# Kernel optimization log

Measured on AMD Instinct MI355X. Metric: run time of the kernel, lower is better.

The kernel has to match this reference:

```python
import jax, jax.numpy as jnp
import numpy as np

T = 4096          # total packed tokens
SEG = 512         # segment length (position_ids reset every SEG)
D = 768           # hidden_size
H = 12            # num_attention_heads
DH = D // H       # head_dim = 64
THETA = 160000.0  # global_rope_theta (layer_id=0 -> global attention)


def setup_inputs() -> dict:
    key = jax.random.key(0)
    k1, k2, k3 = jax.random.split(key, 3)
    hidden_states = jax.random.normal(k1, (T, D), dtype=jnp.float32)
    # torch Linear weights stored transposed: here [in, out] for x @ W
    Wqkv = jax.random.normal(k2, (D, 3 * D), dtype=jnp.float32) / np.sqrt(D).astype(np.float32)
    Wo = jax.random.normal(k3, (D, D), dtype=jnp.float32) / np.sqrt(D).astype(np.float32)
    # packed batch: 8 segments of length SEG, position ids restart at 0
    position_ids = (jnp.arange(T, dtype=jnp.int32) % SEG)
    return {"hidden_states": hidden_states, "Wqkv": Wqkv, "Wo": Wo,
            "position_ids": position_ids}


def _neox_rope(x, pos):
    # x: [T, H, DH]; neox-style rotary over full head_dim
    half = DH // 2
    inv_freq = 1.0 / (THETA ** (jnp.arange(half, dtype=jnp.float32) * 2.0 / DH))
    freqs = pos.astype(jnp.float32)[:, None] * inv_freq[None, :]   # [T, half]
    cos = jnp.cos(freqs)[:, None, :]                               # [T, 1, half]
    sin = jnp.sin(freqs)[:, None, :]
    x1, x2 = x[..., :half], x[..., half:]
    return jnp.concatenate([x1 * cos - x2 * sin, x2 * cos + x1 * sin], axis=-1)


def reference(hidden_states, Wqkv, Wo, position_ids):
    qkv = hidden_states @ Wqkv                         # [T, 3D]
    q, k, v = jnp.split(qkv, 3, axis=-1)
    q = q.reshape(T, H, DH)
    k = k.reshape(T, H, DH)
    v = v.reshape(T, H, DH)
    q = _neox_rope(q, position_ids)
    k = _neox_rope(k, position_ids)
    # segment id per token (position_ids==0 marks a new sequence)
    seg = jnp.cumsum((position_ids == 0).astype(jnp.int32)) - 1
    mask = seg[:, None] == seg[None, :]                # block-diagonal [T, T]
    scale = 1.0 / np.sqrt(DH).astype(np.float32)
    scores = jnp.einsum('thd,shd->hts', q, k) * scale  # [H, T, T]
    scores = jnp.where(mask[None, :, :], scores, jnp.float32(-1e30))
    attn = jax.nn.softmax(scores, axis=-1)
    out = jnp.einsum('hts,shd->thd', attn, v).reshape(T, D)
    return out @ Wo
```

## Files before the change

### kernel.cpp

```cpp
#include <hip/hip_runtime.h>
#include <hip/hip_bf16.h>
#include <math.h>

#define T_TOK 4096
#define D_MODEL 768
#define H_HEADS 12
#define DH 64
#define SEG 512
#define NSEG 8
#define QKV_LD 2304

typedef __bf16 bf16x8_t __attribute__((ext_vector_type(8)));
typedef float f32x4_t __attribute__((ext_vector_type(4)));
typedef float f32x16_t __attribute__((ext_vector_type(16)));

#define GBK 64
#define QSCALE 0.18033688011112042f

#define FENCED_BARRIER()                         \
    do {                                         \
        __builtin_amdgcn_sched_barrier(0);       \
        __builtin_amdgcn_s_barrier();            \
        __builtin_amdgcn_sched_barrier(0);       \
    } while (0)

__device__ __forceinline__ void tconv_body(const float* __restrict__ in,
                                           __hip_bfloat16* __restrict__ out,
                                           int N, int K, int bx, int by, int tid,
                                           float (*tile)[65]) {
    const int k0 = by * 64;
    const int n0 = bx * 64;
    const int rr = tid >> 4;
    const int cc = (tid & 15) * 4;
#pragma unroll
    for (int i = 0; i < 4; ++i) {
        int r = i * 16 + rr;
        float4 v = *(const float4*)(in + (size_t)(k0 + r) * N + n0 + cc);
        tile[r][cc] = v.x; tile[r][cc + 1] = v.y; tile[r][cc + 2] = v.z; tile[r][cc + 3] = v.w;
    }
    __syncthreads();
#pragma unroll
    for (int i = 0; i < 4; ++i) {
        int n = i * 16 + rr;
        union { __hip_bfloat16 h[4]; ushort4 u; } o;
        o.h[0] = __float2bfloat16(tile[cc + 0][n]);
        o.h[1] = __float2bfloat16(tile[cc + 1][n]);
        o.h[2] = __float2bfloat16(tile[cc + 2][n]);
        o.h[3] = __float2bfloat16(tile[cc + 3][n]);
        *(ushort4*)(out + (size_t)(n0 + n) * K + k0 + cc) = o.u;
    }
}

__global__ __launch_bounds__(256) void prep_inputs(const float* __restrict__ hidden,
                                                   const float* __restrict__ Wqkv,
                                                   const float* __restrict__ Wo,
                                                   const int* __restrict__ pos_ids,
                                                   __hip_bfloat16* __restrict__ Xb,
                                                   __hip_bfloat16* __restrict__ Wqkvt,
                                                   __hip_bfloat16* __restrict__ Wot,
                                                   float2* __restrict__ rtab) {
    __shared__ float tile[64][65];
    const int b = blockIdx.x;
    const int tid = threadIdx.x;
    if (b < 3072) {
        int i = b * 256 + tid;
        float4 v = ((const float4*)hidden)[i];
        union { __hip_bfloat16 h[4]; ushort4 u; } o;
        o.h[0] = __float2bfloat16(v.x); o.h[1] = __float2bfloat16(v.y);
        o.h[2] = __float2bfloat16(v.z); o.h[3] = __float2bfloat16(v.w);
        ((ushort4*)Xb)[i] = o.u;
    } else if (b < 3504) {
        int lb = b - 3072;
        tconv_body(Wqkv, Wqkvt, QKV_LD, D_MODEL, lb % 36, lb / 36, tid, tile);
    } else if (b < 3648) {
        int lb = b - 3504;
        tconv_body(Wo, Wot, D_MODEL, D_MODEL, lb % 12, lb / 12, tid, tile);
    } else {
        int idx = (b - 3648) * 256 + tid;
        int t = idx >> 5;
        int i = idx & 31;
        float pos = (float)pos_ids[t];
        float inv_freq = powf(160000.0f, -(float)i / 32.0f);
        float s, c;
        sincosf(pos * inv_freq, &s, &c);
        rtab[idx] = make_float2(c, s);
    }
}

__global__ __launch_bounds__(256) void gemm_qkv_fused(const __hip_bfloat16* __restrict__ A,
                                                      const __hip_bfloat16* __restrict__ Bt,
                                                      const float2* __restrict__ rtab,
                                                      __hip_bfloat16* __restrict__ Qb,
                                                      __hip_bfloat16* __restrict__ Kb,
                                                      __hip_bfloat16* __restrict__ Vtb) {
    __shared__ __hip_bfloat16 As[2][64 * GBK];
    __shared__ __hip_bfloat16 Bs[2][128 * GBK];
    const int tid = threadIdx.x;
    const int lane = tid & 63;
    const int wid = tid >> 6;
    const int wr = wid >> 1;
    const int wc = wid & 1;
    const int orig = blockIdx.y * 18 + blockIdx.x;
    const int wg = (orig & 7) * 144 + (orig >> 3);
    const int m0 = (wg / 18) * 64;
    const int n0 = (wg % 18) * 128;
    const int K = D_MODEL;

    f32x4_t acc[2][4];
#pragma unroll
    for (int i = 0; i < 2; ++i)
#pragma unroll
        for (int j = 0; j < 4; ++j) acc[i][j] = (f32x4_t){0.f, 0.f, 0.f, 0.f};

    const int lr = lane >> 3;
    const int gc = lane & 7;
    const int swzc = (gc ^ lr) << 3;
    const int fr = lane & 15;
    const int l4 = lane >> 4;
    const int fsw = fr & 7;

#define STAGE_Q(buf_, k0_)                                                            \
    do {                                                                              \
        _Pragma("unroll")                                                             \
        for (int i_ = 0; i_ < 2; ++i_) {                                              \
            const int row_ = wid * 16 + i_ * 8;                                       \
            const __hip_bfloat16* ga_ = A + (size_t)(m0 + row_ + lr) * K + (k0_) + swzc; \
            __builtin_amdgcn_global_load_lds(                                         \
                (const __attribute__((address_space(1))) void*)ga_,                   \
                (__attribute__((address_space(3))) void*)(As[buf_] + row_ * GBK), 16, 0, 0); \
        }                                                                             \
        _Pragma("unroll")                                                             \
        for (int i_ = 0; i_ < 4; ++i_) {                                              \
            const int row_ = wid * 32 + i_ * 8;                                       \
            const __hip_bfloat16* gb_ = Bt + (size_t)(n0 + row_ + lr) * K + (k0_) + swzc; \
            __builtin_amdgcn_global_load_lds(                                         \
                (const __attribute__((address_space(1))) void*)gb_,                   \
                (__attribute__((address_space(3))) void*)(Bs[buf_] + row_ * GBK), 16, 0, 0); \
        }                                                                             \
    } while (0)

    const int NKT = K / GBK;
    STAGE_Q(0, 0);
    for (int kt = 0; kt < NKT; ++kt) {
        const int cur = kt & 1;
        if (kt < NKT - 1) {
            STAGE_Q(cur ^ 1, (kt + 1) * GBK);
            asm volatile("s_waitcnt vmcnt(6)" ::: "memory");
        } else {
            asm volatile("s_waitcnt vmcnt(0)" ::: "memory");
        }
        FENCED_BARRIER();
#pragma unroll
        for (int kk = 0; kk < 2; ++kk) {
            const int rg = ((kk * 4 + l4) ^ fsw) << 3;
            bf16x8_t af[2], bfr[4];
#pragma unroll
            for (int mi = 0; mi < 2; ++mi)
                af[mi] = *(const bf16x8_t*)(As[cur] + (wr * 32 + mi * 16 + fr) * GBK + rg);
#pragma unroll
            for (int ni = 0; ni < 4; ++ni)
                bfr[ni] = *(const bf16x8_t*)(Bs[cur] + (wc * 64 + ni * 16 + fr) * GBK + rg);
#pragma unroll
            for (int mi = 0; mi < 2; ++mi)
#pragma unroll
                for (int ni = 0; ni < 4; ++ni)
                    acc[mi][ni] = __builtin_amdgcn_mfma_f32_16x16x32_bf16(
                        af[mi], bfr[ni], acc[mi][ni], 0, 0, 0);
        }
        asm volatile("" ::: "memory");
        FENCED_BARRIER();
    }
#undef STAGE_Q

    const int colbase = n0 + wc * 64;
    const int chunk = colbase >> 6;
    const int part = chunk / H_HEADS;
    const int h = chunk % H_HEADS;
    const int trow0 = m0 + wr * 32;

    if (part == 2) {
        const int seg = trow0 >> 9;
        const int key0 = (trow0 & 511) + l4 * 4;
        __hip_bfloat16* vdst = Vtb + ((size_t)(h * NSEG + seg) * DH) * SEG;
#pragma unroll
        for (int mi = 0; mi < 2; ++mi)
#pragma unroll
            for (int ni = 0; ni < 4; ++ni) {
                int d = ni * 16 + fr;
                union { __hip_bfloat16 h2[4]; ushort4 u; } o;
#pragma unroll
                for (int j = 0; j < 4; ++j) o.h2[j] = __float2bfloat16(acc[mi][ni][j]);
                *(ushort4*)(vdst + (size_t)d * SEG + key0 + mi * 16) = o.u;
            }
    } else {
        __hip_bfloat16* dst = (part == 0) ? Qb : Kb;
        const float scale = (part == 0) ? QSCALE : 1.0f;
#pragma unroll
        for (int mi = 0; mi < 2; ++mi)
#pragma unroll
            for (int j = 0; j < 4; ++j) {
                int t = trow0 + mi * 16 + l4 * 4 + j;
                const float2* tb = rtab + (size_t)t * 32;
                float2 cs0 = tb[fr];
                float2 cs1 = tb[16 + fr];
                __hip_bfloat16* op = dst + ((size_t)h * T_TOK + t) * DH;
                float x1, x2;
                x1 = acc[mi][0][j]; x2 = acc[mi][2][j];
                op[fr]      = __float2bfloat16((x1 * cs0.x - x2 * cs0.y) * scale);
                op[fr + 32] = __float2bfloat16((x2 * cs0.x + x1 * cs0.y) * scale);
                x1 = acc[mi][1][j]; x2 = acc[mi][3][j];
                op[16 + fr] = __float2bfloat16((x1 * cs1.x - x2 * cs1.y) * scale);
                op[48 + fr] = __float2bfloat16((x2 * cs1.x + x1 * cs1.y) * scale);
            }
    }
}

__global__ __launch_bounds__(256) void gemm_wo64(const __hip_bfloat16* __restrict__ A,
                                                 const __hip_bfloat16* __restrict__ Bt,
                                                 float* __restrict__ C) {
    __shared__ __hip_bfloat16 As[2][64 * GBK];
    __shared__ __hip_bfloat16 Bs[2][64 * GBK];
    const int tid = threadIdx.x;
    const int lane = tid & 63;
    const int wid = tid >> 6;
    const int wr = wid >> 1, wc = wid & 1;
    const int orig = blockIdx.y * 12 + blockIdx.x;
    const int wg = (orig & 7) * 96 + (orig >> 3);
    const int m0 = (wg / 12) * 64;
    const int n0 = (wg % 12) * 64;
    const int K = D_MODEL;
    const int N = D_MODEL;

    f32x4_t acc[2][2];
#pragma unroll
    for (int i = 0; i < 2; ++i)
#pragma unroll
        for (int j = 0; j < 2; ++j) acc[i][j] = (f32x4_t){0.f, 0.f, 0.f, 0.f};

    const int lr = lane >> 3;
    const int gc = lane & 7;
    const int swzc = (gc ^ lr) << 3;
    const int fr = lane & 15;
    const int l4 = lane >> 4;
    const int fsw = fr & 7;

#define STAGE_W(buf_, k0_)                                                            \
    do {                                                                              \
        _Pragma("unroll")                                                             \
        for (int i_ = 0; i_ < 2; ++i_) {                                              \
            const int row_ = i_ * 32 + wid * 8;                                       \
            const __hip_bfloat16* ga_ = A + (size_t)(m0 + row_ + lr) * K + (k0_) + swzc; \
            __builtin_amdgcn_global_load_lds(                                         \
                (const __attribute__((address_space(1))) void*)ga_,                   \
                (__attribute__((address_space(3))) void*)(As[buf_] + row_ * GBK), 16, 0, 0); \
            const __hip_bfloat16* gb_ = Bt + (size_t)(n0 + row_ + lr) * K + (k0_) + swzc; \
            __builtin_amdgcn_global_load_lds(                                         \
                (const __attribute__((address_space(1))) void*)gb_,                   \
                (__attribute__((address_space(3))) void*)(Bs[buf_] + row_ * GBK), 16, 0, 0); \
        }                                                                             \
    } while (0)

    const int NKT = K / GBK;
    STAGE_W(0, 0);
    for (int kt = 0; kt < NKT; ++kt) {
        const int cur = kt & 1;
        if (kt < NKT - 1) {
            STAGE_W(cur ^ 1, (kt + 1) * GBK);
            asm volatile("s_waitcnt vmcnt(4)" ::: "memory");
        } else {
            asm volatile("s_waitcnt vmcnt(0)" ::: "memory");
        }
        FENCED_BARRIER();
#pragma unroll
        for (int kk = 0; kk < 2; ++kk) {
            const int rg = ((kk * 4 + l4) ^ fsw) << 3;
            bf16x8_t af[2], bfr[2];
#pragma unroll
            for (int mi = 0; mi < 2; ++mi)
                af[mi] = *(const bf16x8_t*)(As[cur] + (wr * 32 + mi * 16 + fr) * GBK + rg);
#pragma unroll
            for (int ni = 0; ni < 2; ++ni)
                bfr[ni] = *(const bf16x8_t*)(Bs[cur] + (wc * 32 + ni * 16 + fr) * GBK + rg);
#pragma unroll
            for (int mi = 0; mi < 2; ++mi)
#pragma unroll
                for (int ni = 0; ni < 2; ++ni)
                    acc[mi][ni] = __builtin_amdgcn_mfma_f32_16x16x32_bf16(
                        af[mi], bfr[ni], acc[mi][ni], 0, 0, 0);
        }
        asm volatile("" ::: "memory");
        FENCED_BARRIER();
    }
#undef STAGE_W

    float* Cb = C + (size_t)(m0 + wr * 32) * N + n0 + wc * 32;
#pragma unroll
    for (int mi = 0; mi < 2; ++mi)
#pragma unroll
        for (int ni = 0; ni < 2; ++ni)
#pragma unroll
            for (int j = 0; j < 4; ++j) {
                int r = mi * 16 + (lane >> 4) * 4 + j;
                Cb[(size_t)r * N + ni * 16 + fr] = acc[mi][ni][j];
            }
}

__device__ __forceinline__ unsigned pk2(float a, float b) {
    unsigned ua = (unsigned)__bfloat16_as_ushort(__float2bfloat16(a));
    unsigned ub = (unsigned)__bfloat16_as_ushort(__float2bfloat16(b));
    return ua | (ub << 16);
}

__global__ __launch_bounds__(256) void attn_mfma(const __hip_bfloat16* __restrict__ Qb,
                                                 const __hip_bfloat16* __restrict__ Kb,
                                                 const __hip_bfloat16* __restrict__ Vtb,
                                                 __hip_bfloat16* __restrict__ attnb) {
    __shared__ __hip_bfloat16 KS[2][64 * 64];
    __shared__ __hip_bfloat16 VS[2][64 * 64];

    const int tid = threadIdx.x;
    const int lane = tid & 63;
    const int w = tid >> 6;
    const int qw = w & 1;
    const int par = w >> 1;
    const int hi = lane >> 5;
    const int l31 = lane & 31;
    const int orig = blockIdx.x;
    const int wg = (orig & 7) * 96 + (orig >> 3);
    const int qt = wg & 7;
    const int hs = wg >> 3;
    const int h = hs % H_HEADS;
    const int seg = hs / H_HEADS;
    const int t0 = seg * SEG + qt * 64 + qw * 32;

    const __hip_bfloat16* kb = Kb + ((size_t)h * T_TOK + seg * SEG) * DH;
    const __hip_bfloat16* vb = Vtb + (size_t)(h * NSEG + seg) * DH * SEG;

    bf16x8_t qf[4];
    {
        const __hip_bfloat16* qp = Qb + ((size_t)h * T_TOK + t0 + l31) * DH + hi * 8;
#pragma unroll
        for (int s = 0; s < 4; ++s) qf[s] = *(const bf16x8_t*)(qp + s * 16);
    }

    const int gr = lane >> 3;
    const int gc = lane & 7;

    f32x16_t ot[2];
#pragma unroll
    for (int n = 0; n < 2; ++n)
#pragma unroll
        for (int r = 0; r < 16; ++r) ot[n][r] = 0.f;
    float lrun = 0.f;

    for (int it = 0; it < 4; ++it) {
        const int tile = 2 * it + par;
#pragma unroll
        for (int i = 0; i < 4; ++i) {
            int G = i * 128 + qw * 64;
            int rk = (G >> 3) + gr;
            const __hip_bfloat16* sk = kb + (size_t)(tile * 64 + rk) * DH + ((gc ^ (rk & 7)) << 3);
            __builtin_amdgcn_global_load_lds(
                (const __attribute__((address_space(1))) void*)sk,
                (__attribute__((address_space(3))) void*)(&KS[par][G * 8]), 16, 0, 0);
            const __hip_bfloat16* sv = vb + (size_t)rk * SEG + tile * 64 + ((gc ^ (rk & 7)) << 3);
            __builtin_amdgcn_global_load_lds(
                (const __attribute__((address_space(1))) void*)sv,
                (__attribute__((address_space(3))) void*)(&VS[par][G * 8]), 16, 0, 0);
        }
        asm volatile("s_waitcnt vmcnt(0)" ::: "memory");
        FENCED_BARRIER();

        f32x16_t st[2];
#pragma unroll
        for (int t = 0; t < 2; ++t)
#pragma unroll
            for (int r = 0; r < 16; ++r) st[t][r] = 0.f;
#pragma unroll
        for (int s = 0; s < 4; ++s) {
            int gk = s * 2 + hi;
            bf16x8_t k0 = *(const bf16x8_t*)(&KS[par][l31 * 64 + ((gk ^ (l31 & 7)) << 3)]);
            bf16x8_t k1 = *(const bf16x8_t*)(&KS[par][(32 + l31) * 64 + ((gk ^ (l31 & 7)) << 3)]);
            st[0] = __builtin_amdgcn_mfma_f32_32x32x16_bf16(k0, qf[s], st[0], 0, 0, 0);
            st[1] = __builtin_amdgcn_mfma_f32_32x32x16_bf16(k1, qf[s], st[1], 0, 0, 0);
        }

        float psum = 0.f;
#pragma unroll
        for (int t = 0; t < 2; ++t)
#pragma unroll
            for (int r = 0; r < 16; ++r) {
                float p = exp2f(st[t][r]);
                st[t][r] = p;
                psum += p;
            }
        psum += __shfl_xor(psum, 32);
        lrun += psum;

        bf16x8_t pf[4];
#pragma unroll
        for (int t = 0; t < 2; ++t) {
            unsigned wv[8], ov[8];
#pragma unroll
            for (int j = 0; j < 8; ++j) wv[j] = pk2(st[t][2 * j], st[t][2 * j + 1]);
#pragma unroll
            for (int j = 0; j < 8; ++j) ov[j] = (unsigned)__shfl_xor((int)wv[j], 32);
#pragma unroll
            for (int sh = 0; sh < 2; ++sh) {
                int b = sh * 4;
                union { unsigned u[4]; bf16x8_t v; } u8;
                u8.u[0] = hi ? ov[b + 2] : wv[b + 0];
                u8.u[1] = hi ? ov[b + 3] : wv[b + 1];
                u8.u[2] = hi ? wv[b + 2] : ov[b + 0];
                u8.u[3] = hi ? wv[b + 3] : ov[b + 1];
                pf[t * 2 + sh] = u8.v;
            }
        }

#pragma unroll
        for (int s = 0; s < 4; ++s) {
            int gk = s * 2 + hi;
            bf16x8_t v0 = *(const bf16x8_t*)(&VS[par][l31 * 64 + ((gk ^ (l31 & 7)) << 3)]);
            bf16x8_t v1 = *(const bf16x8_t*)(&VS[par][(32 + l31) * 64 + ((gk ^ (l31 & 7)) << 3)]);
            ot[0] = __builtin_amdgcn_mfma_f32_32x32x16_bf16(v0, pf[s], ot[0], 0, 0, 0);
            ot[1] = __builtin_amdgcn_mfma_f32_32x32x16_bf16(v1, pf[s], ot[1], 0, 0, 0);
        }
        FENCED_BARRIER();
    }

    float* redO = (float*)KS;
    float* redL = (float*)VS;
    if (par == 1) {
#pragma unroll
        for (int n = 0; n < 2; ++n)
#pragma unroll
            for (int r = 0; r < 16; ++r)
                redO[(qw * 32 + n * 16 + r) * 64 + lane] = ot[n][r];
        redL[qw * 64 + lane] = lrun;
    }
    FENCED_BARRIER();
    if (par == 1) return;
#pragma unroll
    for (int n = 0; n < 2; ++n)
#pragma unroll
        for (int r = 0; r < 16; ++r)
            ot[n][r] += redO[(qw * 32 + n * 16 + r) * 64 + lane];
    lrun += redL[qw * 64 + lane];

    float invl = 1.0f / lrun;
    ushort* Os = (ushort*)VS + 256 + qw * 2112;
#pragma unroll
    for (int n = 0; n < 2; ++n)
#pragma unroll
        for (int r = 0; r < 16; ++r) {
            int d = n * 32 + (r & 3) + 8 * (r >> 2) + 4 * hi;
            Os[d * 33 + l31] = __bfloat16_as_ushort(__float2bfloat16(ot[n][r] * invl));
        }
    {
        unsigned ow2[16];
#pragma unroll
        for (int j = 0; j < 16; ++j) {
            unsigned lo = Os[(hi * 32 + 2 * j) * 33 + l31];
            unsigned hh = Os[(hi * 32 + 2 * j + 1) * 33 + l31];
            ow2[j] = lo | (hh << 16);
        }
        uint4* gd = (uint4*)(attnb + (size_t)(t0 + l31) * D_MODEL + h * DH + hi * 32);
        gd[0] = make_uint4(ow2[0], ow2[1], ow2[2], ow2[3]);
        gd[1] = make_uint4(ow2[4], ow2[5], ow2[6], ow2[7]);
        gd[2] = make_uint4(ow2[8], ow2[9], ow2[10], ow2[11]);
        gd[3] = make_uint4(ow2[12], ow2[13], ow2[14], ow2[15]);
    }
}

extern "C" void kernel_launch(void* const* d_in, const int* in_sizes, int n_in,
                              void* d_out, int out_size, void* d_ws, size_t ws_size,
                              hipStream_t stream) {
    const float* hidden = (const float*)d_in[0];
    const float* Wqkv   = (const float*)d_in[1];
    const float* Wo     = (const float*)d_in[2];
    const int*   pos    = (const int*)d_in[3];

    char* ws = (char*)d_ws;
    __hip_bfloat16* Xb    = (__hip_bfloat16*)(ws);
    __hip_bfloat16* Wqkvt = (__hip_bfloat16*)(ws + 6291456);
    __hip_bfloat16* Wot   = (__hip_bfloat16*)(ws + 9830400);
    __hip_bfloat16* Qb    = (__hip_bfloat16*)(ws + 11010048);
    __hip_bfloat16* Kb    = (__hip_bfloat16*)(ws + 17301504);
    __hip_bfloat16* Vtb   = (__hip_bfloat16*)(ws + 23592960);
    __hip_bfloat16* attnb = (__hip_bfloat16*)(ws + 29884416);
    float2* rtab          = (float2*)(ws + 36175872);
    float* out = (float*)d_out;

    prep_inputs<<<4160, 256, 0, stream>>>(hidden, Wqkv, Wo, pos, Xb, Wqkvt, Wot, rtab);

    gemm_qkv_fused<<<dim3(18, T_TOK / 64), 256, 0, stream>>>(
        Xb, Wqkvt, rtab, Qb, Kb, Vtb);

    attn_mfma<<<768, 256, 0, stream>>>(Qb, Kb, Vtb, attnb);

    gemm_wo64<<<dim3(D_MODEL / 64, T_TOK / 64), 256, 0, stream>>>(
        attnb, Wot, out);
}
```

Measured before the change: 65.87 us.

## Load QKV GEMM A-fragments directly from global into registers, bypassing LDS

```diff
diff --git a/kernel.cpp b/kernel.cpp
--- a/kernel.cpp
+++ b/kernel.cpp
@@ -93,7 +93,6 @@
                                                       __hip_bfloat16* __restrict__ Qb,
                                                       __hip_bfloat16* __restrict__ Kb,
                                                       __hip_bfloat16* __restrict__ Vtb) {
-    __shared__ __hip_bfloat16 As[2][64 * GBK];
     __shared__ __hip_bfloat16 Bs[2][128 * GBK];
     const int tid = threadIdx.x;
     const int lane = tid & 63;
@@ -119,16 +118,19 @@
     const int l4 = lane >> 4;
     const int fsw = fr & 7;
 
-#define STAGE_Q(buf_, k0_)                                                            \
+    const __hip_bfloat16* a0 = A + (size_t)(m0 + wr * 32 + fr) * K + l4 * 8;
+    const __hip_bfloat16* a1 = a0 + (size_t)16 * K;
+
+#define LOAD_AF(dst_, kt_)                                            \
+    do {                                                              \
+        dst_[0][0] = *(const bf16x8_t*)(a0 + (kt_) * GBK);            \
+        dst_[0][1] = *(const bf16x8_t*)(a0 + (kt_) * GBK + 32);       \
+        dst_[1][0] = *(const bf16x8_t*)(a1 + (kt_) * GBK);            \
+        dst_[1][1] = *(const bf16x8_t*)(a1 + (kt_) * GBK + 32);       \
+    } while (0)
+
+#define STAGE_B(buf_, k0_)                                                            \
     do {                                                                              \
-        _Pragma("unroll")                                                             \
-        for (int i_ = 0; i_ < 2; ++i_) {                                              \
-            const int row_ = wid * 16 + i_ * 8;                                       \
-            const __hip_bfloat16* ga_ = A + (size_t)(m0 + row_ + lr) * K + (k0_) + swzc; \
-            __builtin_amdgcn_global_load_lds(                                         \
-                (const __attribute__((address_space(1))) void*)ga_,                   \
-                (__attribute__((address_space(3))) void*)(As[buf_] + row_ * GBK), 16, 0, 0); \
-        }                                                                             \
         _Pragma("unroll")                                                             \
         for (int i_ = 0; i_ < 4; ++i_) {                                              \
             const int row_ = wid * 32 + i_ * 8;                                       \
@@ -139,38 +141,56 @@
         }                                                                             \
     } while (0)
 
-    const int NKT = K / GBK;
-    STAGE_Q(0, 0);
-    for (int kt = 0; kt < NKT; ++kt) {
-        const int cur = kt & 1;
-        if (kt < NKT - 1) {
-            STAGE_Q(cur ^ 1, (kt + 1) * GBK);
-            asm volatile("s_waitcnt vmcnt(6)" ::: "memory");
+#define MFMA_STEP(afx_, cur_)                                                         \
+    do {                                                                              \
+        _Pragma("unroll")                                                             \
+        for (int kk = 0; kk < 2; ++kk) {                                              \
+            const int rg = ((kk * 4 + l4) ^ fsw) << 3;                                \
+            bf16x8_t bfr[4];                                                          \
+            _Pragma("unroll")                                                         \
+            for (int ni = 0; ni < 4; ++ni)                                            \
+                bfr[ni] = *(const bf16x8_t*)(Bs[cur_] + (wc * 64 + ni * 16 + fr) * GBK + rg); \
+            _Pragma("unroll")                                                         \
+            for (int mi = 0; mi < 2; ++mi)                                            \
+                _Pragma("unroll")                                                     \
+                for (int ni = 0; ni < 4; ++ni)                                        \
+                    acc[mi][ni] = __builtin_amdgcn_mfma_f32_16x16x32_bf16(            \
+                        afx_[mi][kk], bfr[ni], acc[mi][ni], 0, 0, 0);                 \
+        }                                                                             \
+    } while (0)
+
+    bf16x8_t afA[2][2], afB[2][2];
+    LOAD_AF(afA, 0);
+    STAGE_B(0, 0);
+#pragma unroll
+    for (int kt = 0; kt < 12; ++kt) {
+        if ((kt & 1) == 0) {
+            if (kt < 11) {
+                LOAD_AF(afB, kt + 1);
+                STAGE_B((kt + 1) & 1, (kt + 1) * GBK);
+                asm volatile("s_waitcnt vmcnt(8)" ::: "memory");
+            } else {
+                asm volatile("s_waitcnt vmcnt(0)" ::: "memory");
+            }
+            FENCED_BARRIER();
+            MFMA_STEP(afA, kt & 1);
         } else {
-            asm volatile("s_waitcnt vmcnt(0)" ::: "memory");
-        }
-        FENCED_BARRIER();
-#pragma unroll
-        for (int kk = 0; kk < 2; ++kk) {
-            const int rg = ((kk * 4 + l4) ^ fsw) << 3;
-            bf16x8_t af[2], bfr[4];
-#pragma unroll
-            for (int mi = 0; mi < 2; ++mi)
-                af[mi] = *(const bf16x8_t*)(As[cur] + (wr * 32 + mi * 16 + fr) * GBK + rg);
-#pragma unroll
-            for (int ni = 0; ni < 4; ++ni)
-                bfr[ni] = *(const bf16x8_t*)(Bs[cur] + (wc * 64 + ni * 16 + fr) * GBK + rg);
-#pragma unroll
-            for (int mi = 0; mi < 2; ++mi)
-#pragma unroll
-                for (int ni = 0; ni < 4; ++ni)
-                    acc[mi][ni] = __builtin_amdgcn_mfma_f32_16x16x32_bf16(
-                        af[mi], bfr[ni], acc[mi][ni], 0, 0, 0);
+            if (kt < 11) {
+                LOAD_AF(afA, kt + 1);
+                STAGE_B((kt + 1) & 1, (kt + 1) * GBK);
+                asm volatile("s_waitcnt vmcnt(8)" ::: "memory");
+            } else {
+                asm volatile("s_waitcnt vmcnt(0)" ::: "memory");
+            }
+            FENCED_BARRIER();
+            MFMA_STEP(afB, kt & 1);
         }
         asm volatile("" ::: "memory");
         FENCED_BARRIER();
     }
-#undef STAGE_Q
+#undef LOAD_AF
+#undef STAGE_B
+#undef MFMA_STEP
 
     const int colbase = n0 + wc * 64;
     const int chunk = colbase >> 6;
```

Measured after the change: 81.18 us. 1.23x slower.
